# Kernel tuning notes

Measured on AMD Instinct MI355X. Metric: run time of the kernel, lower is better.

Reference implementation:

```python
import jax, jax.numpy as jnp
import numpy as np

B, EMBED, H, W = 2, 32, 96, 96
SQ = (4, 2); R = 2; EXP = 2
SCH = EMBED // SQ[0]            # 8  squeezed channel dim
SHSP = SCH * R * R              # 32 shuffled spatial dim
SSP = SHSP // SQ[1]             # 16 squeezed spatial dim (attention embed dim)
HEADS = SCH * EXP               # 16
EACH = SSP // SCH               # 2
IDX = np.array([i + j * SCH for i in range(SCH) for j in range(EACH)])
NIDX = np.array([i + j * EACH for i in range(EACH) for j in range(SCH)])


def conv(x, w, b, stride=1, pad=0, groups=1):
    y = jax.lax.conv_general_dilated(x, w, (stride, stride), [(pad, pad), (pad, pad)],
                                     feature_group_count=groups,
                                     dimension_numbers=('NCHW', 'OIHW', 'NCHW'))
    return y + b[None, :, None, None]


def ln_ch(x, w, b):
    # LayerNorm over channel dim (torch applies it on [B,HW,C])
    mu = x.mean(1, keepdims=True)
    var = ((x - mu) ** 2).mean(1, keepdims=True)
    return (x - mu) * jax.lax.rsqrt(var + 1e-5) * w[None, :, None, None] + b[None, :, None, None]


def l2n(x, axis):
    # F.normalize: divide by L2 norm clamped to eps
    return x / jnp.maximum(jnp.sqrt(jnp.sum(x * x, axis=axis, keepdims=True)), 1e-12)


def _qkv(x, wqkv, bqkv):
    Bb, C, Hh, Ww = x.shape
    qkv = conv(x, wqkv, bqkv, groups=C)                        # [B, C*EXP*3, H, W], per-channel 1x1
    qkv = qkv.reshape(Bb, C, EXP * 3, Hh, Ww).transpose(0, 2, 1, 3, 4)
    q, k, v = jnp.split(qkv, 3, axis=1)                        # each [B, EXP, C, H, W]
    hd = EXP * C // HEADS
    rs = lambda a: a.reshape(Bb, HEADS, hd, Hh * Ww)
    return rs(q), rs(k), rs(v)


def _fuse(o, wfus, bfus, Bb, C, Hh, Ww):
    o = o.reshape(Bb, EXP, C, Hh, Ww).transpose(0, 2, 1, 3, 4).reshape(Bb, C * EXP, Hh, Ww)
    return conv(o, wfus, bfus, groups=C)


def chan_attn(x, wqkv, bqkv, t, wfus, bfus):
    Bb, C, Hh, Ww = x.shape
    q, k, v = _qkv(x, wqkv, bqkv)
    q, k = l2n(q, -1), l2n(k, -1)
    a = jax.nn.softmax(jnp.einsum('bhdn,bhen->bhde', q, k) * t, axis=-1)   # [B,h,d,d]
    o = jnp.einsum('bhde,bhen->bhdn', a, v)
    return _fuse(o, wfus, bfus, Bb, C, Hh, Ww)


def spat_attn(x, wqkv, bqkv, t, wfus, bfus):
    Bb, C, Hh, Ww = x.shape
    q, k, v = _qkv(x, wqkv, bqkv)
    q, k = l2n(q, -2), l2n(k, -2)
    a = jax.nn.softmax(jnp.einsum('bhdn,bhdm->bhnm', q, k) * t, axis=-1)   # [B,h,HW,HW]
    o = jnp.einsum('bhnm,bhdm->bhdn', a, v)
    return _fuse(o, wfus, bfus, Bb, C, Hh, Ww)


def pixel_shuffle(x, r):
    Bb, C, Hh, Ww = x.shape
    x = x.reshape(Bb, C // (r * r), r, r, Hh, Ww).transpose(0, 1, 4, 2, 5, 3)
    return x.reshape(Bb, C // (r * r), Hh * r, Ww * r)


def _forward(x, ln1_w, ln1_b, cab_w1, cab_b1, cab_w2, cab_b2, cab_aw1, cab_ab1, cab_aw2, cab_ab2,
             sq1_w, sq1_b, sq2_w, sq2_b, ca_qkv_w, ca_qkv_b, ca_t, ca_fus_w, ca_fus_b,
             sa_qkv_w, sa_qkv_b, sa_t, sa_fus_w, sa_fus_b, un1_w, un1_b, un2_w, un2_b,
             ln2_w, ln2_b, da_w1, da_b1, da_dw_w, da_dw_b, da_pw, da_pb):
    Bb, C, Hh, Ww = x.shape
    xn = ln_ch(x, ln1_w, ln1_b)
    # ---- CAB branch (conv-GELU-conv + RCAN channel attention) ----
    c = jax.nn.gelu(conv(xn, cab_w1, cab_b1, pad=1), approximate=False)
    c = conv(c, cab_w2, cab_b2, pad=1)
    y = c.mean((2, 3), keepdims=True)
    y = jax.nn.relu(conv(y, cab_aw1, cab_ab1))
    y = jax.nn.sigmoid(conv(y, cab_aw2, cab_ab2))
    x_cab = c * y
    # ---- Condensed attention branch ----
    z = conv(xn, sq1_w, sq1_b)                                   # 1x1: C -> SCH
    z = conv(z, sq2_w, sq2_b, stride=R, groups=SCH)              # grouped RxR stride R: -> [B,SSP,H/R,W/R]
    z = z[:, IDX]
    z = chan_attn(z, ca_qkv_w, ca_qkv_b, ca_t, ca_fus_w, ca_fus_b)
    z = z[:, NIDX]
    z = spat_attn(z, sa_qkv_w, sa_qkv_b, sa_t, sa_fus_w, sa_fus_b)
    z = conv(z, un1_w, un1_b, groups=SCH)                        # SSP -> SHSP
    z = pixel_shuffle(z, R)                                      # -> [B,SCH,H,W]
    z = conv(z, un2_w, un2_b)                                    # SCH -> C
    x = x + z + x_cab
    # ---- Dual adaptive (gated depthwise-conv FFN) ----
    xn2 = ln_ch(x, ln2_w, ln2_b)
    d = conv(xn2, da_w1, da_b1)
    d = conv(d, da_dw_w, da_dw_b, pad=3, groups=C).reshape(Bb, C, 2, Hh, Ww)
    d = jax.nn.gelu(d[:, :, 0], approximate=False) * jax.nn.sigmoid(d[:, :, 1])
    d = conv(d, da_pw, da_pb)
    return x + d


def setup_inputs():
    key = jax.random.key(0)
    ks = iter(jax.random.split(key, 40))
    nrm = lambda s: jax.random.normal(next(ks), s, jnp.float32) * 0.05
    inp = {'x': jax.random.normal(next(ks), (B, EMBED, H, W), jnp.float32)}
    wshapes = {
        'cab_w1': (EMBED // 4, EMBED, 3, 3), 'cab_w2': (EMBED, EMBED // 4, 3, 3),
        'cab_aw1': (EMBED // 18, EMBED, 1, 1), 'cab_aw2': (EMBED, EMBED // 18, 1, 1),
        'sq1_w': (SCH, EMBED, 1, 1), 'sq2_w': (SSP, 1, R, R),
        'ca_qkv_w': (SSP * EXP * 3, 1, 1, 1), 'ca_fus_w': (SSP, EXP, 1, 1),
        'sa_qkv_w': (SSP * EXP * 3, 1, 1, 1), 'sa_fus_w': (SSP, EXP, 1, 1),
        'un1_w': (SHSP, SSP // SCH, 1, 1), 'un2_w': (EMBED, SCH, 1, 1),
        'da_w1': (EMBED, EMBED, 1, 1), 'da_dw_w': (2 * EMBED, 1, 7, 7), 'da_pw': (EMBED, EMBED, 1, 1),
    }
    bshapes = {'cab_b1': EMBED // 4, 'cab_b2': EMBED, 'cab_ab1': EMBED // 18, 'cab_ab2': EMBED,
               'sq1_b': SCH, 'sq2_b': SSP, 'ca_qkv_b': SSP * EXP * 3, 'ca_fus_b': SSP,
               'sa_qkv_b': SSP * EXP * 3, 'sa_fus_b': SSP, 'un1_b': SHSP, 'un2_b': EMBED,
               'da_b1': EMBED, 'da_dw_b': 2 * EMBED, 'da_pb': EMBED}
    for n, s in wshapes.items():
        inp[n] = nrm(s)
    for n, s in bshapes.items():
        inp[n] = nrm((s,))
    inp['ln1_w'] = jnp.ones((EMBED,), jnp.float32); inp['ln1_b'] = jnp.zeros((EMBED,), jnp.float32)
    inp['ln2_w'] = jnp.ones((EMBED,), jnp.float32); inp['ln2_b'] = jnp.zeros((EMBED,), jnp.float32)
    inp['ca_t'] = jnp.ones((1, HEADS, 1, 1), jnp.float32)
    inp['sa_t'] = jnp.ones((1, HEADS, 1, 1), jnp.float32)
    return inp


def reference(x, ln1_w, ln1_b, cab_w1, cab_b1, cab_w2, cab_b2, cab_aw1, cab_ab1, cab_aw2, cab_ab2,
              sq1_w, sq1_b, sq2_w, sq2_b, ca_qkv_w, ca_qkv_b, ca_t, ca_fus_w, ca_fus_b,
              sa_qkv_w, sa_qkv_b, sa_t, sa_fus_w, sa_fus_b, un1_w, un1_b, un2_w, un2_b,
              ln2_w, ln2_b, da_w1, da_b1, da_dw_w, da_dw_b, da_pw, da_pb):
    return _forward(x, ln1_w, ln1_b, cab_w1, cab_b1, cab_w2, cab_b2, cab_aw1, cab_ab1, cab_aw2, cab_ab2,
                    sq1_w, sq1_b, sq2_w, sq2_b, ca_qkv_w, ca_qkv_b, ca_t, ca_fus_w, ca_fus_b,
                    sa_qkv_w, sa_qkv_b, sa_t, sa_fus_w, sa_fus_b, un1_w, un1_b, un2_w, un2_b,
                    ln2_w, ln2_b, da_w1, da_b1, da_dw_w, da_dw_b, da_pw, da_pb)
```

## Files before the change

### kernel.cpp

```cpp
#include <hip/hip_runtime.h>
#include <cstdint>
#include <math.h>

#define NP 9216
#define NP2 2304
#define KH 12
#define NMOM 78

__device__ __forceinline__ float gelu_ex(float v){
  return 0.5f*v*(1.0f+erff(v*0.70710678118654752440f));
}
__device__ __forceinline__ float sigm(float v){
  return 1.0f/(1.0f+__expf(-v));
}

__global__ __launch_bounds__(256) void k_ln1(const float* __restrict__ x,
    const float* __restrict__ lw, const float* __restrict__ lb,
    const float* __restrict__ sw, const float* __restrict__ sb,
    float* __restrict__ xn, float* __restrict__ z1)
{
  __shared__ float sred[2][8][32];
  __shared__ float xnsh[32][33];
  int p = threadIdx.x & 31, sl = threadIdx.x >> 5;
  int pix = blockIdx.x*32 + p;
  int b = pix / NP, n = pix % NP;
  const float* xp = x + (size_t)b*32*NP + (size_t)(sl*4)*NP + n;
  float v[4]; float s=0.f, s2=0.f;
#pragma unroll
  for (int c=0;c<4;c++){ float t=xp[(size_t)c*NP]; v[c]=t; s+=t; s2+=t*t; }
  sred[0][sl][p]=s; sred[1][sl][p]=s2;
  __syncthreads();
  s=0.f; s2=0.f;
#pragma unroll
  for (int g=0;g<8;g++){ s += sred[0][g][p]; s2 += sred[1][g][p]; }
  float mu = s*(1.f/32.f);
  float var = s2*(1.f/32.f)-mu*mu;
  float rs = rsqrtf(var+1e-5f);
  float* xo = xn + (size_t)b*32*NP + (size_t)(sl*4)*NP + n;
#pragma unroll
  for (int c=0;c<4;c++){
    int cc = sl*4+c;
    float t = (v[c]-mu)*rs*lw[cc]+lb[cc];
    xo[(size_t)c*NP] = t;
    xnsh[p][cc] = t;
  }
  __syncthreads();
  float vv[32];
#pragma unroll
  for (int c=0;c<32;c++) vv[c]=xnsh[p][c];
  int g = sl;
  float a = sb[g];
#pragma unroll
  for (int c=0;c<32;c++) a += vv[c]*sw[g*32+c];
  z1[(size_t)b*8*NP + (size_t)g*NP + n] = a;
}

__global__ __launch_bounds__(256) void k_cab1(const float* __restrict__ xn,
    const float* __restrict__ w, const float* __restrict__ bias,
    float* __restrict__ c1)
{
  int og = blockIdx.x/72, pb = blockIdx.x%72;
  int idx = pb*256+threadIdx.x;
  int b = idx/NP, n = idx%NP, i = n/96, j = n%96;
  const float* xb = xn + (size_t)b*32*NP;
  const float* wb = w + og*288;
  int  o_[9]; float m_[9];
  int d=0;
#pragma unroll
  for (int di=0;di<3;di++){
    int ii=i+di-1; bool vi = (unsigned)ii<96u;
#pragma unroll
    for (int dj=0;dj<3;dj++){
      int jj=j+dj-1; bool v = vi && ((unsigned)jj<96u);
      o_[d] = v ? ii*96+jj : 0; m_[d] = v ? 1.f : 0.f; d++;
    }
  }
  float accd[9] = {0,0,0,0,0,0,0,0,0};
  for (int c=0;c<32;c++){
    const float* xp = xb + (size_t)c*NP;
    const float* wp = wb + c*9;
    float t[9];
#pragma unroll
    for (int d2=0;d2<9;d2++) t[d2] = xp[o_[d2]];
#pragma unroll
    for (int d2=0;d2<9;d2++) accd[d2] += t[d2]*wp[d2];
  }
  float acc = bias[og];
#pragma unroll
  for (int d2=0;d2<9;d2++) acc += accd[d2]*m_[d2];
  c1[(size_t)b*8*NP + (size_t)og*NP + n] = gelu_ex(acc);
}

__global__ __launch_bounds__(256) void k_cab2(const float* __restrict__ c1,
    const float* __restrict__ w, const float* __restrict__ bias,
    float* __restrict__ cbuf, float* __restrict__ ypart)
{
  int og = blockIdx.x/72, pb = blockIdx.x%72;
  int idx = pb*256+threadIdx.x;
  int b = idx/NP, n = idx%NP, i = n/96, j = n%96;
  const float* cb = c1 + (size_t)b*8*NP;
  int  o_[9]; float m_[9];
  int d=0;
#pragma unroll
  for (int di=0;di<3;di++){
    int ii=i+di-1; bool vi = (unsigned)ii<96u;
#pragma unroll
    for (int dj=0;dj<3;dj++){
      int jj=j+dj-1; bool v = vi && ((unsigned)jj<96u);
      o_[d] = v ? ii*96+jj : 0; m_[d] = v ? 1.f : 0.f; d++;
    }
  }
  float acc[4];
#pragma unroll
  for (int k=0;k<4;k++) acc[k]=bias[og*4+k];
  for (int c=0;c<8;c++){
    const float* xp = cb + (size_t)c*NP;
    float t[9];
#pragma unroll
    for (int d2=0;d2<9;d2++) t[d2] = xp[o_[d2]]*m_[d2];
#pragma unroll
    for (int k=0;k<4;k++){
      const float* wp = w + (og*4+k)*72 + c*9;
#pragma unroll
      for (int d2=0;d2<9;d2++) acc[k] += t[d2]*wp[d2];
    }
  }
  __shared__ float red[4][4];
  int wv = threadIdx.x>>6, ln = threadIdx.x&63;
#pragma unroll
  for (int k=0;k<4;k++){
    cbuf[(size_t)b*32*NP + (size_t)(og*4+k)*NP + n] = acc[k];
    float r = acc[k];
#pragma unroll
    for (int m=1;m<64;m<<=1) r += __shfl_xor(r, m, 64);
    if (ln==0) red[wv][k]=r;
  }
  __syncthreads();
  if (threadIdx.x<4){
    float r = red[0][threadIdx.x]+red[1][threadIdx.x]+red[2][threadIdx.x]+red[3][threadIdx.x];
    ypart[(og*72+pb)*4 + threadIdx.x] = r;
  }
}

__global__ __launch_bounds__(256) void k_sq2(const float* __restrict__ z1,
    const float* __restrict__ w, const float* __restrict__ bias,
    float* __restrict__ u, float* __restrict__ spart)
{
  int pr = blockIdx.x/18, pb = blockIdx.x%18;
  int idx = pb*256+threadIdx.x;
  int b = idx/NP2, n = idx%NP2, i = n/48, j = n%48;
  int ocA = pr, ocB = pr+8;
  int gA = ocA>>1, gB = ocB>>1;
  const float* zpA = z1 + ((size_t)b*8+gA)*NP + (size_t)(2*i)*96 + 2*j;
  const float* zpB = z1 + ((size_t)b*8+gB)*NP + (size_t)(2*i)*96 + 2*j;
  float vA = zpA[0]*w[ocA*4]+zpA[1]*w[ocA*4+1]+zpA[96]*w[ocA*4+2]+zpA[97]*w[ocA*4+3]+bias[ocA];
  float vB = zpB[0]*w[ocB*4]+zpB[1]*w[ocB*4+1]+zpB[96]*w[ocB*4+2]+zpB[97]*w[ocB*4+3]+bias[ocB];
  u[((size_t)b*16+2*pr)*NP2 + n]   = vA;
  u[((size_t)b*16+2*pr+1)*NP2 + n] = vB;
  __shared__ float red[4][5];
  int wv=threadIdx.x>>6, ln=threadIdx.x&63;
  float st[5]={vA,vB,vA*vA,vB*vB,vA*vB};
#pragma unroll
  for (int k=0;k<5;k++){
    float r=st[k];
#pragma unroll
    for (int m=1;m<64;m<<=1) r+=__shfl_xor(r,m,64);
    if (ln==0) red[wv][k]=r;
  }
  __syncthreads();
  if (threadIdx.x<5){
    float r = red[0][threadIdx.x]+red[1][threadIdx.x]+red[2][threadIdx.x]+red[3][threadIdx.x];
    spart[(b*9 + (pb%9))*40 + pr*5 + threadIdx.x] = r;
  }
}

__global__ __launch_bounds__(256) void k_qkmom(const float* __restrict__ u,
    const float* __restrict__ spart,
    const float* __restrict__ cqw, const float* __restrict__ cqb,
    const float* __restrict__ cat, const float* __restrict__ cfw,
    const float* __restrict__ cfb,
    const float* __restrict__ qw, const float* __restrict__ qb,
    float2* __restrict__ qarr, float* __restrict__ mompart)
{
  int bh = blockIdx.x/9, ch = blockIdx.x%9;
  int n = ch*256 + threadIdx.x;
  int b = bh>>4, h = bh&15;
  int p = h&7, s = h>>3;
  int cc0=2*p, cc1=2*p+1;
  int oc0 = 2*(cc0&7)+(cc0>>3);
  int oc1 = 2*(cc1&7)+(cc1>>3);
  float AA[2], BB[2], CCc[2];
#pragma unroll
  for (int t2=0;t2<2;t2++){
    int oc = t2? oc1:oc0;
    int p2 = oc>>1, dd = oc&1;
    float st[5]={0,0,0,0,0};
    for (int ib=0; ib<9; ib++){
#pragma unroll
      for (int k=0;k<5;k++) st[k] += spart[(b*9+ib)*40 + p2*5 + k];
    }
    float S0=st[0],S1=st[1],Q00=st[2],Q11=st[3],Q01=st[4];
    float Sd = dd? S1:S0;
    float Qdd = dd? Q11:Q00;
    float cu0[2],cu1[2],ccst[2];
#pragma unroll
    for (int hh=0;hh<2;hh++){
      int h2=p2+8*hh;
      float th2=cat[h2];
      float aq=cqw[(2*p2+dd)*6+hh], bq=cqb[(2*p2+dd)*6+hh];
      float nq=fmaxf(sqrtf(fmaxf(aq*aq*Qdd+2.f*aq*bq*Sd+2304.f*bq*bq,0.f)),1e-12f);
      float m2[2],av[2],bv[2];
#pragma unroll
      for (int e=0;e<2;e++){
        float Se_=e?S1:S0, Qee=e?Q11:Q00, Qde=(dd==e)?Qdd:Q01;
        float ak=cqw[(2*p2+e)*6+2+hh], bk=cqb[(2*p2+e)*6+2+hh];
        float nk=fmaxf(sqrtf(fmaxf(ak*ak*Qee+2.f*ak*bk*Se_+2304.f*bk*bk,0.f)),1e-12f);
        float D=aq*ak*Qde + aq*bk*Sd + bq*ak*Se_ + 2304.f*bq*bk;
        m2[e]=th2*D/(nq*nk);
        av[e]=cqw[(2*p2+e)*6+4+hh]; bv[e]=cqb[(2*p2+e)*6+4+hh];
      }
      float mx=fmaxf(m2[0],m2[1]);
      float e0=__expf(m2[0]-mx), e1=__expf(m2[1]-mx);
      float inv=1.f/(e0+e1);
      cu0[hh]=e0*inv*av[0]; cu1[hh]=e1*inv*av[1]; ccst[hh]=e0*inv*bv[0]+e1*inv*bv[1];
    }
    float f0=cfw[oc*2], f1=cfw[oc*2+1];
    AA[t2]=f0*cu0[0]+f1*cu0[1];
    BB[t2]=f0*cu1[0]+f1*cu1[1];
    CCc[t2]=f0*ccst[0]+f1*ccst[1]+cfb[oc];
  }
  const float* u00 = u + ((size_t)b*16 + (oc0>>1)*2)*NP2;
  const float* u01 = u00 + NP2;
  const float* u10 = u + ((size_t)b*16 + (oc1>>1)*2)*NP2;
  const float* u11 = u10 + NP2;
  float w0 = AA[0]*u00[n]+BB[0]*u01[n]+CCc[0];
  float w1 = AA[1]*u10[n]+BB[1]*u11[n]+CCc[1];
  float k0 = qw[cc0*6+2+s]*w0+qb[cc0*6+2+s];
  float k1 = qw[cc1*6+2+s]*w1+qb[cc1*6+2+s];
  float rnk = 1.f/fmaxf(sqrtf(k0*k0+k1*k1),1e-12f);
  float kc = k0*rnk, ks = k1*rnk;
  float q0 = qw[cc0*6+s]*w0+qb[cc0*6+s];
  float q1 = qw[cc1*6+s]*w1+qb[cc1*6+s];
  float rnq = 1.f/fmaxf(sqrtf(q0*q0+q1*q1),1e-12f);
  qarr[bh*NP2+n] = make_float2(q0*rnq, q1*rnq);

  __shared__ float red[16][80];
  int grp = threadIdx.x>>4, gl = threadIdx.x&15;
  float c = 1.f, sn = 0.f;
#pragma unroll
  for (int k=0;k<=KH;k++){
    float vals[6] = {c, sn, c*w0, sn*w0, c*w1, sn*w1};
#pragma unroll
    for (int j=0;j<6;j++){
      float r = vals[j];
      r += __shfl_xor(r, 1, 64);
      r += __shfl_xor(r, 2, 64);
      r += __shfl_xor(r, 4, 64);
      r += __shfl_xor(r, 8, 64);
      if (gl==0) red[grp][k*6+j] = r;
    }
    float cn = c*kc - sn*ks;
    sn = sn*kc + c*ks;
    c = cn;
  }
  __syncthreads();
  if (threadIdx.x < NMOM){
    float r = 0.f;
#pragma unroll
    for (int g=0;g<16;g++) r += red[g][threadIdx.x];
    mompart[(bh*9+ch)*NMOM + threadIdx.x] = r;
  }
}

__global__ __launch_bounds__(256) void k_rows(const float2* __restrict__ qarr,
    const float* __restrict__ mompart, const float* __restrict__ sat,
    const float* __restrict__ qw, const float* __restrict__ qb,
    const float* __restrict__ fw, const float* __restrict__ fb,
    const float* __restrict__ u1w, const float* __restrict__ u1b,
    float* __restrict__ ps)
{
  int bp = blockIdx.x/9, ch = blockIdx.x%9;
  int b = bp>>3, p = bp&7;
  int n = ch*256 + (int)threadIdx.x;
  __shared__ float msh[2][80];
  __shared__ float fsh[2][13];
  int tid = threadIdx.x;
  if (tid < 26){
    int hh = tid/13, k = tid%13;
    double t = (double)sat[p+8*hh];
    double fac;
    if (fabs(t) < 1e-3){
      double xh = 0.5*t;
      double pk = 1.0;
      for (int q=1;q<=k;q++) pk *= xh/(double)q;
      double Ik = pk*(1.0 + xh*xh/(double)(k+1));
      fac = (k? 2.0:1.0)*Ik;
    } else {
      const int KS = 36;
      double ip1 = 0.0, ik = 1e-280, sum2 = 0.0;
      double vk = 0.0, v0 = 0.0;
      for (int q=KS; q>=1; --q){
        if (q == k) vk = ik;
        sum2 += ik;
        double im1 = ip1 + (2.0*(double)q/t)*ik;
        ip1 = ik; ik = im1;
      }
      v0 = ik;
      if (k == 0) vk = v0;
      double total = v0 + 2.0*sum2;
      double scale = exp(t)/total;
      fac = (k? 2.0:1.0)*vk*scale;
    }
    fsh[hh][k] = (float)fac;
  }
  if (tid < 2*NMOM){
    int hh = tid/NMOM, jj = tid%NMOM;
    float ssum = 0.f;
    for (int ib=0; ib<9; ib++)
      ssum += mompart[((size_t)(b*16+p+8*hh)*9+ib)*NMOM + jj];
    msh[hh][jj] = ssum;
  }
  __syncthreads();
  if (tid < 2*NMOM){
    int hh = tid/NMOM, jj = tid%NMOM;
    msh[hh][jj] *= fsh[hh][jj/6];
  }
  __syncthreads();
  float o[2][2];
#pragma unroll
  for (int hh=0;hh<2;hh++){
    float2 q = qarr[(size_t)(b*16+p+8*hh)*NP2 + n];
    float c = 1.f, sn = 0.f;
    float Se=0.f, S0=0.f, S1=0.f;
#pragma unroll
    for (int k=0;k<=KH;k++){
      const float* mk = &msh[hh][k*6];
      Se += c*mk[0] + sn*mk[1];
      S0 += c*mk[2] + sn*mk[3];
      S1 += c*mk[4] + sn*mk[5];
      float cn = c*q.x - sn*q.y;
      sn = sn*q.x + c*q.y;
      c = cn;
    }
    float rSe = 1.f/Se;
    float av0=qw[(2*p)*6+4+hh],  bv0=qb[(2*p)*6+4+hh];
    float av1=qw[(2*p+1)*6+4+hh],bv1=qb[(2*p+1)*6+4+hh];
    o[hh][0]=av0*S0*rSe+bv0;
    o[hh][1]=av1*S1*rSe+bv1;
  }
  float zz0 = o[0][0]*fw[(2*p)*2]   + o[1][0]*fw[(2*p)*2+1]   + fb[2*p];
  float zz1 = o[0][1]*fw[(2*p+1)*2] + o[1][1]*fw[(2*p+1)*2+1] + fb[2*p+1];
  int i=n/48, j=n%48;
  float* pb = ps + ((size_t)b*8+p)*NP;
#pragma unroll
  for (int k=0;k<4;k++){
    int od = 4*p+k;
    float v = zz0*u1w[od*2] + zz1*u1w[od*2+1] + u1b[od];
    pb[(size_t)(2*i+(k>>1))*96 + 2*j + (k&1)] = v;
  }
}

__global__ __launch_bounds__(256) void k_un2(const float* __restrict__ ps,
    const float* __restrict__ ypart,
    const float* __restrict__ aw1, const float* __restrict__ ab1,
    const float* __restrict__ aw2, const float* __restrict__ ab2,
    const float* __restrict__ u2w, const float* __restrict__ u2b,
    const float* __restrict__ x, const float* __restrict__ cbuf,
    const float* __restrict__ lw, const float* __restrict__ lb,
    const float* __restrict__ dw1, const float* __restrict__ db1,
    float* __restrict__ xsum, float* __restrict__ d1)
{
  __shared__ float sred[2][8][32];
  __shared__ float xsh[32][33];
  __shared__ float y2sh[32];
  int p = threadIdx.x & 31, sl = threadIdx.x >> 5;
  int pix = blockIdx.x*32 + p;
  int b = pix/NP, n = pix%NP;
  if (threadIdx.x < 32){
    int c = threadIdx.x;
    float ssum = 0.f;
    for (int ib=0; ib<36; ib++)
      ssum += ypart[((c>>2)*72 + b*36 + ib)*4 + (c&3)];
    float pr = ssum*(1.f/9216.f)*aw1[c];
#pragma unroll
    for (int m=1;m<32;m<<=1) pr += __shfl_xor(pr, m, 64);
    float y1 = fmaxf(pr+ab1[0], 0.f);
    y2sh[c] = sigm(aw2[c]*y1+ab2[c]);
  }
  float pg[8];
#pragma unroll
  for (int g=0;g<8;g++) pg[g]=ps[((size_t)b*8+g)*NP+n];
  __syncthreads();
  float xv[4]; float s=0.f,s2=0.f;
#pragma unroll
  for (int c=0;c<4;c++){
    int cc = sl*4+c;
    float a=u2b[cc];
#pragma unroll
    for (int g=0;g<8;g++) a+=pg[g]*u2w[cc*8+g];
    size_t off=((size_t)b*32+cc)*NP+n;
    float t = x[off]+a+cbuf[off]*y2sh[cc];
    xv[c]=t; xsum[off]=t; s+=t; s2+=t*t;
  }
  sred[0][sl][p]=s; sred[1][sl][p]=s2;
  __syncthreads();
  s=0.f; s2=0.f;
#pragma unroll
  for (int g=0;g<8;g++){ s += sred[0][g][p]; s2 += sred[1][g][p]; }
  float mu=s*(1.f/32.f), var=s2*(1.f/32.f)-mu*mu, rs=rsqrtf(var+1e-5f);
#pragma unroll
  for (int c=0;c<4;c++){
    int cc = sl*4+c;
    xsh[p][cc] = (xv[c]-mu)*rs*lw[cc]+lb[cc];
  }
  __syncthreads();
  float vv[32];
#pragma unroll
  for (int c=0;c<32;c++) vv[c]=xsh[p][c];
#pragma unroll
  for (int k=0;k<4;k++){
    int o = sl*4+k;
    float a=db1[o];
#pragma unroll
    for (int cc=0;cc<32;cc++) a+=vv[cc]*dw1[o*32+cc];
    d1[((size_t)b*32+o)*NP+n]=a;
  }
}

__global__ __launch_bounds__(256) void k_dw(const float* __restrict__ d1,
    const float* __restrict__ w, const float* __restrict__ bias,
    float* __restrict__ dg)
{
  int idx = blockIdx.x*256+threadIdx.x;
  int pl = idx/4608, n2 = idx%4608;
  int i2 = n2/96, j = n2%96;
  int c = pl&31;
  const float* dp = d1 + (size_t)pl*NP;
  const float* w0p = w + (2*c)*49;
  const float* w1p = w + (2*c+1)*49;
  float a0=bias[2*c], a1=bias[2*c+1];
  float c0=bias[2*c], c1=bias[2*c+1];
#pragma unroll
  for (int di=0;di<8;di++){
    int ii=2*i2-3+di; if ((unsigned)ii>=96u) continue;
    const float* rowp = dp + ii*96;
    float t[7];
#pragma unroll
    for (int dj=0;dj<7;dj++){
      int jj=j+dj-3;
      t[dj] = ((unsigned)jj<96u) ? rowp[jj] : 0.f;
    }
    if (di<7){
#pragma unroll
      for (int dj=0;dj<7;dj++){ a0 += t[dj]*w0p[di*7+dj]; a1 += t[dj]*w1p[di*7+dj]; }
    }
    if (di>0){
#pragma unroll
      for (int dj=0;dj<7;dj++){ c0 += t[dj]*w0p[(di-1)*7+dj]; c1 += t[dj]*w1p[(di-1)*7+dj]; }
    }
  }
  dg[(size_t)pl*NP + (size_t)(2*i2)*96 + j]   = gelu_ex(a0)*sigm(a1);
  dg[(size_t)pl*NP + (size_t)(2*i2+1)*96 + j] = gelu_ex(c0)*sigm(c1);
}

__global__ __launch_bounds__(256) void k_fin(const float* __restrict__ dg,
    const float* __restrict__ pw, const float* __restrict__ pb,
    const float* __restrict__ xsum, float* __restrict__ out)
{
  __shared__ float xsh[32][33];
  int p = threadIdx.x & 31, sl = threadIdx.x >> 5;
  int pix = blockIdx.x*32 + p;
  int b = pix/NP, n = pix%NP;
  const float* dp = dg + ((size_t)b*32 + sl*4)*NP + n;
#pragma unroll
  for (int c=0;c<4;c++) xsh[p][sl*4+c]=dp[(size_t)c*NP];
  __syncthreads();
  float vv[32];
#pragma unroll
  for (int c=0;c<32;c++) vv[c]=xsh[p][c];
#pragma unroll
  for (int k=0;k<4;k++){
    int o = sl*4+k;
    float a=pb[o];
#pragma unroll
    for (int cc=0;cc<32;cc++) a+=vv[cc]*pw[o*32+cc];
    size_t off=((size_t)b*32+o)*NP+n;
    out[off]=xsum[off]+a;
  }
}

extern "C" void kernel_launch(void* const* d_in, const int* in_sizes, int n_in,
                              void* d_out, int out_size, void* d_ws, size_t ws_size,
                              hipStream_t stream) {
  (void)in_sizes; (void)n_in; (void)out_size; (void)ws_size;
  const float* x       =(const float*)d_in[0];
  const float* cab_w1  =(const float*)d_in[1];
  const float* cab_w2  =(const float*)d_in[2];
  const float* cab_aw1 =(const float*)d_in[3];
  const float* cab_aw2 =(const float*)d_in[4];
  const float* sq1_w   =(const float*)d_in[5];
  const float* sq2_w   =(const float*)d_in[6];
  const float* ca_qkv_w=(const float*)d_in[7];
  const float* ca_fus_w=(const float*)d_in[8];
  const float* sa_qkv_w=(const float*)d_in[9];
  const float* sa_fus_w=(const float*)d_in[10];
  const float* un1_w   =(const float*)d_in[11];
  const float* un2_w   =(const float*)d_in[12];
  const float* da_w1   =(const float*)d_in[13];
  const float* da_dw_w =(const float*)d_in[14];
  const float* da_pw   =(const float*)d_in[15];
  const float* cab_b1  =(const float*)d_in[16];
  const float* cab_b2  =(const float*)d_in[17];
  const float* cab_ab1 =(const float*)d_in[18];
  const float* cab_ab2 =(const float*)d_in[19];
  const float* sq1_b   =(const float*)d_in[20];
  const float* sq2_b   =(const float*)d_in[21];
  const float* ca_qkv_b=(const float*)d_in[22];
  const float* ca_fus_b=(const float*)d_in[23];
  const float* sa_qkv_b=(const float*)d_in[24];
  const float* sa_fus_b=(const float*)d_in[25];
  const float* un1_b   =(const float*)d_in[26];
  const float* un2_b   =(const float*)d_in[27];
  const float* da_b1   =(const float*)d_in[28];
  const float* da_dw_b =(const float*)d_in[29];
  const float* da_pb   =(const float*)d_in[30];
  const float* ln1_w   =(const float*)d_in[31];
  const float* ln1_b   =(const float*)d_in[32];
  const float* ln2_w   =(const float*)d_in[33];
  const float* ln2_b   =(const float*)d_in[34];
  const float* ca_t    =(const float*)d_in[35];
  const float* sa_t    =(const float*)d_in[36];

  float* ws=(float*)d_ws;
  float* xn    = ws;
  float* z1    = ws + 589824;
  float* c1b   = ws + 737280;
  float* cb    = ws + 884736;
  float* u     = ws + 1474560;
  float* psb   = ws + 1548288;
  float* xsm   = ws + 1695744;
  float* ypart = ws + 2285568;
  float* spart = ws + 2287872;
  float2* qarr = (float2*)(ws + 2288640);
  float* mompart = ws + 2436096;
  float* d1    = xn;
  float* dg    = cb;

  k_ln1  <<<576, 256,0,stream>>>(x, ln1_w, ln1_b, sq1_w, sq1_b, xn, z1);
  k_cab1 <<<576, 256,0,stream>>>(xn, cab_w1, cab_b1, c1b);
  k_cab2 <<<576, 256,0,stream>>>(c1b, cab_w2, cab_b2, cb, ypart);
  k_sq2  <<<144, 256,0,stream>>>(z1, sq2_w, sq2_b, u, spart);
  k_qkmom<<<288, 256,0,stream>>>(u, spart, ca_qkv_w, ca_qkv_b, ca_t, ca_fus_w, ca_fus_b,
                                 sa_qkv_w, sa_qkv_b, qarr, mompart);
  k_rows <<<144, 256,0,stream>>>(qarr, mompart, sa_t, sa_qkv_w, sa_qkv_b,
                                 sa_fus_w, sa_fus_b, un1_w, un1_b, psb);
  k_un2  <<<576, 256,0,stream>>>(psb, ypart, cab_aw1, cab_ab1, cab_aw2, cab_ab2,
                                 un2_w, un2_b, x, cb, ln2_w, ln2_b, da_w1, da_b1, xsm, d1);
  k_dw   <<<1152,256,0,stream>>>(d1, da_dw_w, da_dw_b, dg);
  k_fin  <<<576, 256,0,stream>>>(dg, da_pw, da_pb, xsm, (float*)d_out);
}
```

Measured before the change: 86.11 us.

## Split conv input channels across waves and fuse depthwise conv with pointwise output

The two 3x3 conv kernels now give each block 64 pixels and split input channels across its four waves. Each thread computes every output channel and the partial sums are reduced through shared memory, so each input neighbourhood is loaded once instead of once per output group. The ypart channel-mean partials are laid out per block and summed accordingly. The depthwise 7x7 gated conv is fused with the final pointwise 1x1 projection and residual add, which removes the dg intermediate buffer and one kernel launch. The cost is more registers (32 accumulators in cab2), larger shared memory and fewer blocks for the conv kernels.

```diff
diff --git a/kernel.cpp b/kernel.cpp
--- a/kernel.cpp
+++ b/kernel.cpp
@@ -59,11 +59,10 @@
     const float* __restrict__ w, const float* __restrict__ bias,
     float* __restrict__ c1)
 {
-  int og = blockIdx.x/72, pb = blockIdx.x%72;
-  int idx = pb*256+threadIdx.x;
+  __shared__ float red[4][64][9];
+  int p = threadIdx.x & 63, sl = threadIdx.x >> 6;
+  int idx = blockIdx.x*64 + p;
   int b = idx/NP, n = idx%NP, i = n/96, j = n%96;
-  const float* xb = xn + (size_t)b*32*NP;
-  const float* wb = w + og*288;
   int  o_[9]; float m_[9];
   int d=0;
 #pragma unroll
@@ -75,30 +74,40 @@
       o_[d] = v ? ii*96+jj : 0; m_[d] = v ? 1.f : 0.f; d++;
     }
   }
-  float accd[9] = {0,0,0,0,0,0,0,0,0};
-  for (int c=0;c<32;c++){
+  const float* xb = xn + (size_t)b*32*NP + (size_t)(sl*8)*NP;
+  float acc8[8] = {0,0,0,0,0,0,0,0};
+#pragma unroll
+  for (int c=0;c<8;c++){
     const float* xp = xb + (size_t)c*NP;
-    const float* wp = wb + c*9;
     float t[9];
 #pragma unroll
-    for (int d2=0;d2<9;d2++) t[d2] = xp[o_[d2]];
-#pragma unroll
-    for (int d2=0;d2<9;d2++) accd[d2] += t[d2]*wp[d2];
-  }
-  float acc = bias[og];
-#pragma unroll
-  for (int d2=0;d2<9;d2++) acc += accd[d2]*m_[d2];
-  c1[(size_t)b*8*NP + (size_t)og*NP + n] = gelu_ex(acc);
+    for (int d2=0;d2<9;d2++) t[d2] = xp[o_[d2]]*m_[d2];
+    const float* wp = w + (sl*8+c)*9;
+#pragma unroll
+    for (int o=0;o<8;o++){
+#pragma unroll
+      for (int d2=0;d2<9;d2++) acc8[o] += t[d2]*wp[o*288+d2];
+    }
+  }
+#pragma unroll
+  for (int o=0;o<8;o++) red[sl][p][o] = acc8[o];
+  __syncthreads();
+#pragma unroll
+  for (int k=0;k<2;k++){
+    int o = sl*2+k;
+    float a = bias[o] + red[0][p][o]+red[1][p][o]+red[2][p][o]+red[3][p][o];
+    c1[(size_t)b*8*NP + (size_t)o*NP + n] = gelu_ex(a);
+  }
 }
 
 __global__ __launch_bounds__(256) void k_cab2(const float* __restrict__ c1,
     const float* __restrict__ w, const float* __restrict__ bias,
     float* __restrict__ cbuf, float* __restrict__ ypart)
 {
-  int og = blockIdx.x/72, pb = blockIdx.x%72;
-  int idx = pb*256+threadIdx.x;
+  __shared__ float red[4][64][33];
+  int p = threadIdx.x & 63, sl = threadIdx.x >> 6;
+  int idx = blockIdx.x*64 + p;
   int b = idx/NP, n = idx%NP, i = n/96, j = n%96;
-  const float* cb = c1 + (size_t)b*8*NP;
   int  o_[9]; float m_[9];
   int d=0;
 #pragma unroll
@@ -110,35 +119,40 @@
       o_[d] = v ? ii*96+jj : 0; m_[d] = v ? 1.f : 0.f; d++;
     }
   }
-  float acc[4];
-#pragma unroll
-  for (int k=0;k<4;k++) acc[k]=bias[og*4+k];
-  for (int c=0;c<8;c++){
-    const float* xp = cb + (size_t)c*NP;
+  const float* cbp = c1 + (size_t)b*8*NP + (size_t)(sl*2)*NP;
+  float acc[32];
+#pragma unroll
+  for (int o=0;o<32;o++) acc[o]=0.f;
+#pragma unroll
+  for (int c=0;c<2;c++){
+    const float* xp = cbp + (size_t)c*NP;
     float t[9];
 #pragma unroll
     for (int d2=0;d2<9;d2++) t[d2] = xp[o_[d2]]*m_[d2];
-#pragma unroll
-    for (int k=0;k<4;k++){
-      const float* wp = w + (og*4+k)*72 + c*9;
-#pragma unroll
-      for (int d2=0;d2<9;d2++) acc[k] += t[d2]*wp[d2];
-    }
-  }
-  __shared__ float red[4][4];
-  int wv = threadIdx.x>>6, ln = threadIdx.x&63;
-#pragma unroll
-  for (int k=0;k<4;k++){
-    cbuf[(size_t)b*32*NP + (size_t)(og*4+k)*NP + n] = acc[k];
-    float r = acc[k];
+    const float* wp = w + (sl*2+c)*9;
+#pragma unroll
+    for (int o=0;o<32;o++){
+#pragma unroll
+      for (int d2=0;d2<9;d2++) acc[o] += t[d2]*wp[o*72+d2];
+    }
+  }
+#pragma unroll
+  for (int o=0;o<32;o++) red[sl][p][o]=acc[o];
+  __syncthreads();
+  float fin[8];
+#pragma unroll
+  for (int k=0;k<8;k++){
+    int o = sl*8+k;
+    float a = bias[o] + red[0][p][o]+red[1][p][o]+red[2][p][o]+red[3][p][o];
+    fin[k]=a;
+    cbuf[(size_t)b*32*NP + (size_t)o*NP + n] = a;
+  }
+#pragma unroll
+  for (int k=0;k<8;k++){
+    float r = fin[k];
 #pragma unroll
     for (int m=1;m<64;m<<=1) r += __shfl_xor(r, m, 64);
-    if (ln==0) red[wv][k]=r;
-  }
-  __syncthreads();
-  if (threadIdx.x<4){
-    float r = red[0][threadIdx.x]+red[1][threadIdx.x]+red[2][threadIdx.x]+red[3][threadIdx.x];
-    ypart[(og*72+pb)*4 + threadIdx.x] = r;
+    if ((threadIdx.x&63)==0) ypart[blockIdx.x*32 + sl*8 + k] = r;
   }
 }
 
@@ -379,8 +393,8 @@
   if (threadIdx.x < 32){
     int c = threadIdx.x;
     float ssum = 0.f;
-    for (int ib=0; ib<36; ib++)
-      ssum += ypart[((c>>2)*72 + b*36 + ib)*4 + (c&3)];
+    for (int ib=0; ib<144; ib++)
+      ssum += ypart[(b*144 + ib)*32 + c];
     float pr = ssum*(1.f/9216.f)*aw1[c];
 #pragma unroll
     for (int m=1;m<32;m<<=1) pr += __shfl_xor(pr, m, 64);
@@ -427,19 +441,21 @@
   }
 }
 
-__global__ __launch_bounds__(256) void k_dw(const float* __restrict__ d1,
+__global__ __launch_bounds__(256) void k_dwfin(const float* __restrict__ d1,
     const float* __restrict__ w, const float* __restrict__ bias,
-    float* __restrict__ dg)
-{
-  int idx = blockIdx.x*256+threadIdx.x;
-  int pl = idx/4608, n2 = idx%4608;
-  int i2 = n2/96, j = n2%96;
-  int c = pl&31;
-  const float* dp = d1 + (size_t)pl*NP;
+    const float* __restrict__ pw, const float* __restrict__ pb,
+    const float* __restrict__ xsum, float* __restrict__ out)
+{
+  __shared__ float g[2][32][9];
+  int bid = blockIdx.x;
+  int jg = bid%12, i2 = (bid/12)%48, b = bid/(12*48);
+  int jj = threadIdx.x&7, c = threadIdx.x>>3;
+  int j = jg*8+jj;
+  const float* dp = d1 + ((size_t)b*32+c)*NP;
   const float* w0p = w + (2*c)*49;
   const float* w1p = w + (2*c+1)*49;
   float a0=bias[2*c], a1=bias[2*c+1];
-  float c0=bias[2*c], c1=bias[2*c+1];
+  float e0=bias[2*c], e1=bias[2*c+1];
 #pragma unroll
   for (int di=0;di<8;di++){
     int ii=2*i2-3+di; if ((unsigned)ii>=96u) continue;
@@ -447,8 +463,8 @@
     float t[7];
 #pragma unroll
     for (int dj=0;dj<7;dj++){
-      int jj=j+dj-3;
-      t[dj] = ((unsigned)jj<96u) ? rowp[jj] : 0.f;
+      int jc=j+dj-3;
+      t[dj] = ((unsigned)jc<96u) ? rowp[jc] : 0.f;
     }
     if (di<7){
 #pragma unroll
@@ -456,36 +472,22 @@
     }
     if (di>0){
 #pragma unroll
-      for (int dj=0;dj<7;dj++){ c0 += t[dj]*w0p[(di-1)*7+dj]; c1 += t[dj]*w1p[(di-1)*7+dj]; }
-    }
-  }
-  dg[(size_t)pl*NP + (size_t)(2*i2)*96 + j]   = gelu_ex(a0)*sigm(a1);
-  dg[(size_t)pl*NP + (size_t)(2*i2+1)*96 + j] = gelu_ex(c0)*sigm(c1);
-}
-
-__global__ __launch_bounds__(256) void k_fin(const float* __restrict__ dg,
-    const float* __restrict__ pw, const float* __restrict__ pb,
-    const float* __restrict__ xsum, float* __restrict__ out)
-{
-  __shared__ float xsh[32][33];
-  int p = threadIdx.x & 31, sl = threadIdx.x >> 5;
-  int pix = blockIdx.x*32 + p;
-  int b = pix/NP, n = pix%NP;
-  const float* dp = dg + ((size_t)b*32 + sl*4)*NP + n;
-#pragma unroll
-  for (int c=0;c<4;c++) xsh[p][sl*4+c]=dp[(size_t)c*NP];
-  __syncthreads();
-  float vv[32];
-#pragma unroll
-  for (int c=0;c<32;c++) vv[c]=xsh[p][c];
-#pragma unroll
-  for (int k=0;k<4;k++){
-    int o = sl*4+k;
-    float a=pb[o];
-#pragma unroll
-    for (int cc=0;cc<32;cc++) a+=vv[cc]*pw[o*32+cc];
-    size_t off=((size_t)b*32+o)*NP+n;
-    out[off]=xsum[off]+a;
+      for (int dj=0;dj<7;dj++){ e0 += t[dj]*w0p[(di-1)*7+dj]; e1 += t[dj]*w1p[(di-1)*7+dj]; }
+    }
+  }
+  g[0][c][jj] = gelu_ex(a0)*sigm(a1);
+  g[1][c][jj] = gelu_ex(e0)*sigm(e1);
+  __syncthreads();
+  float pwr[32];
+#pragma unroll
+  for (int cc=0;cc<32;cc++) pwr[cc]=pw[c*32+cc];
+#pragma unroll
+  for (int r=0;r<2;r++){
+    float a = pb[c];
+#pragma unroll
+    for (int cc=0;cc<32;cc++) a += g[r][cc][jj]*pwr[cc];
+    size_t off = ((size_t)b*32+c)*NP + (size_t)(2*i2+r)*96 + j;
+    out[off] = xsum[off] + a;
   }
 }
 
@@ -540,15 +542,14 @@
   float* psb   = ws + 1548288;
   float* xsm   = ws + 1695744;
   float* ypart = ws + 2285568;
-  float* spart = ws + 2287872;
-  float2* qarr = (float2*)(ws + 2288640);
-  float* mompart = ws + 2436096;
+  float* spart = ws + 2294784;
+  float2* qarr = (float2*)(ws + 2295552);
+  float* mompart = ws + 2443008;
   float* d1    = xn;
-  float* dg    = cb;
 
   k_ln1  <<<576, 256,0,stream>>>(x, ln1_w, ln1_b, sq1_w, sq1_b, xn, z1);
-  k_cab1 <<<576, 256,0,stream>>>(xn, cab_w1, cab_b1, c1b);
-  k_cab2 <<<576, 256,0,stream>>>(c1b, cab_w2, cab_b2, cb, ypart);
+  k_cab1 <<<288, 256,0,stream>>>(xn, cab_w1, cab_b1, c1b);
+  k_cab2 <<<288, 256,0,stream>>>(c1b, cab_w2, cab_b2, cb, ypart);
   k_sq2  <<<144, 256,0,stream>>>(z1, sq2_w, sq2_b, u, spart);
   k_qkmom<<<288, 256,0,stream>>>(u, spart, ca_qkv_w, ca_qkv_b, ca_t, ca_fus_w, ca_fus_b,
                                  sa_qkv_w, sa_qkv_b, qarr, mompart);
@@ -556,6 +557,5 @@
                                  sa_fus_w, sa_fus_b, un1_w, un1_b, psb);
   k_un2  <<<576, 256,0,stream>>>(psb, ypart, cab_aw1, cab_ab1, cab_aw2, cab_ab2,
                                  un2_w, un2_b, x, cb, ln2_w, ln2_b, da_w1, da_b1, xsm, d1);
-  k_dw   <<<1152,256,0,stream>>>(d1, da_dw_w, da_dw_b, dg);
-  k_fin  <<<576, 256,0,stream>>>(dg, da_pw, da_pb, xsm, (float*)d_out);
-}
+  k_dwfin<<<1152,256,0,stream>>>(d1, da_dw_w, da_dw_b, da_pw, da_pb, xsm, (float*)d_out);
+}
```

New measurement: 95.22 us. +10.6%, slower.
